# Kernel tuning notes

Hardware: AMD Instinct MI355X
Metric: run time of the kernel (lower is better)

Reference implementation:

```python
import jax, jax.numpy as jnp
import numpy as np

TEMPERATURE = 0.05
EPS = 1e-8  # torch.cosine_similarity eps


def setup_inputs() -> dict:
    key = jax.random.key(0)
    k1, k2 = jax.random.split(key)
    N, D = 8192, 256
    text_embeddings = jax.random.normal(k1, (N, D), dtype=jnp.float32)
    text_pos_embeddings = jax.random.normal(k2, (N, D), dtype=jnp.float32)
    return {"text_embeddings": text_embeddings, "text_pos_embeddings": text_pos_embeddings}


def reference(text_embeddings, text_pos_embeddings):
    # cosine similarity via normalize + single GEMM (same math as broadcasted
    # torch.cosine_similarity, which clamps norms at eps)
    a_norm = jnp.maximum(jnp.linalg.norm(text_embeddings, axis=-1, keepdims=True), EPS)
    b_norm = jnp.maximum(jnp.linalg.norm(text_pos_embeddings, axis=-1, keepdims=True), EPS)
    a = text_embeddings / a_norm  # [N, D]
    b = text_pos_embeddings / b_norm  # [N, D]
    sim = jnp.einsum("nd,md->nm", a, b) / TEMPERATURE  # [N, N]
    # cross-entropy with labels = arange(N): mean over rows of -log_softmax diag
    logp = jax.nn.log_softmax(sim, axis=-1)
    loss = -jnp.mean(jnp.diagonal(logp))
    return loss
```

## Files before the change

### kernel.cpp

```cpp
#include <hip/hip_runtime.h>
#include <math.h>

#define DIM 256

typedef float f32x4 __attribute__((ext_vector_type(4)));
typedef int   i32x8 __attribute__((ext_vector_type(8)));

__constant__ const float kTempInvLog2e = 20.0f * 1.4426950408889634f;
#define LN2 0.6931471805599453f
#define EPS_NORM 1e-8f
#define SCALE_ONE 0x7F7F7F7Fu

static __device__ inline unsigned f2fp8x4(float4 v, float s) {
    int r = 0;
    r = __builtin_amdgcn_cvt_pk_fp8_f32(v.x * s, v.y * s, r, false);
    r = __builtin_amdgcn_cvt_pk_fp8_f32(v.z * s, v.w * s, r, true);
    return (unsigned)r;
}

static __device__ inline i32x8 mk_frag(uint4 a, uint4 b) {
    i32x8 v;
    v[0] = a.x; v[1] = a.y; v[2] = a.z; v[3] = a.w;
    v[4] = b.x; v[5] = b.y; v[6] = b.z; v[7] = b.w;
    return v;
}

__global__ __launch_bounds__(256) void normpack_kernel(
    const float* __restrict__ A, const float* __restrict__ B,
    unsigned char* __restrict__ Apk, unsigned char* __restrict__ Bpk,
    float* __restrict__ diag, float* __restrict__ rowsum,
    unsigned* __restrict__ counter, int n)
{
    __shared__ uint4 lA[256];
    __shared__ uint4 lB[256];
    const int t = threadIdx.x;
    const int rl = t >> 4;
    const int c16 = t & 15;
    const int r = blockIdx.x * 16 + rl;

    if (blockIdx.x == 0 && t == 0) counter[0] = 0;

    const float4* pa = (const float4*)(A + (size_t)r * DIM + c16 * 16);
    const float4* pb = (const float4*)(B + (size_t)r * DIM + c16 * 16);
    float4 a0 = pa[0], a1 = pa[1], a2 = pa[2], a3 = pa[3];
    float4 b0 = pb[0], b1 = pb[1], b2 = pb[2], b3 = pb[3];

    float ssa = a0.x*a0.x + a0.y*a0.y + a0.z*a0.z + a0.w*a0.w
              + a1.x*a1.x + a1.y*a1.y + a1.z*a1.z + a1.w*a1.w
              + a2.x*a2.x + a2.y*a2.y + a2.z*a2.z + a2.w*a2.w
              + a3.x*a3.x + a3.y*a3.y + a3.z*a3.z + a3.w*a3.w;
    float ssb = b0.x*b0.x + b0.y*b0.y + b0.z*b0.z + b0.w*b0.w
              + b1.x*b1.x + b1.y*b1.y + b1.z*b1.z + b1.w*b1.w
              + b2.x*b2.x + b2.y*b2.y + b2.z*b2.z + b2.w*b2.w
              + b3.x*b3.x + b3.y*b3.y + b3.z*b3.z + b3.w*b3.w;
    float dd  = a0.x*b0.x + a0.y*b0.y + a0.z*b0.z + a0.w*b0.w
              + a1.x*b1.x + a1.y*b1.y + a1.z*b1.z + a1.w*b1.w
              + a2.x*b2.x + a2.y*b2.y + a2.z*b2.z + a2.w*b2.w
              + a3.x*b3.x + a3.y*b3.y + a3.z*b3.z + a3.w*b3.w;
#pragma unroll
    for (int m = 1; m < 16; m <<= 1) {
        ssa += __shfl_xor(ssa, m, 64);
        ssb += __shfl_xor(ssb, m, 64);
        dd  += __shfl_xor(dd, m, 64);
    }
    float na = fmaxf(sqrtf(ssa), EPS_NORM);
    float nb = fmaxf(sqrtf(ssb), EPS_NORM);
    float sa = kTempInvLog2e / na;
    float sb = 1.0f / nb;
    if (c16 == 0) {
        diag[r] = dd / (na * nb) * kTempInvLog2e;
        rowsum[r] = 0.0f;
    }

    const int u = ((c16 >> 3) << 7) + ((c16 & 1) << 6) + rl + ((c16 & 7) >> 1) * 16;
    uint4 ga, gb;
    ga.x = f2fp8x4(a0, sa); ga.y = f2fp8x4(a1, sa);
    ga.z = f2fp8x4(a2, sa); ga.w = f2fp8x4(a3, sa);
    gb.x = f2fp8x4(b0, sb); gb.y = f2fp8x4(b1, sb);
    gb.z = f2fp8x4(b2, sb); gb.w = f2fp8x4(b3, sb);
    lA[u] = ga; lB[u] = gb;
    __syncthreads();

    ((uint4*)Apk)[(size_t)blockIdx.x * 256 + t] = lA[t];
    ((uint4*)Bpk)[(size_t)blockIdx.x * 256 + t] = lB[t];
}

__global__ __launch_bounds__(256, 2) void gemm_lse_kernel(
    const unsigned char* __restrict__ Apk, const unsigned char* __restrict__ Bpk,
    float* __restrict__ rowsum, const float* __restrict__ diag,
    unsigned* __restrict__ counter, float* __restrict__ out, int n)
{
    const int t = threadIdx.x;
    const int lane = t & 63;
    const int w = t >> 6;
    const int c = lane & 15;
    const int q = lane >> 4;

    const int i = blockIdx.x;
    const int split = ((i & 7) << 1) | ((i >> 3) & 1);
    const int rowblk = i >> 4;
    const int rowbase = rowblk * 256 + w * 64;

    i32x8 afrag[4][2];
#pragma unroll
    for (int m = 0; m < 4; ++m) {
        const int AT = rowblk * 16 + w * 4 + m;
#pragma unroll
        for (int kc = 0; kc < 2; ++kc) {
            const char* base = (const char*)Apk + ((size_t)AT * 2 + kc) * 2048 + lane * 16;
            afrag[m][kc] = mk_frag(*(const uint4*)base, *(const uint4*)(base + 1024));
        }
    }
#pragma unroll
    for (int m = 0; m < 4; ++m)
#pragma unroll
        for (int kc = 0; kc < 2; ++kc)
            asm volatile("" : "+v"(afrag[m][kc]));

    float sums[16];
#pragma unroll
    for (int s = 0; s < 16; ++s) sums[s] = 0.0f;

    const char* bb = (const char*)Bpk + (size_t)split * 32 * 4096 + (size_t)lane * 16;

#define LOADT(BUF, IT) do {                                                  \
    _Pragma("unroll") for (int j = 0; j < 8; ++j)                            \
        BUF[j] = *(const uint4*)(bb + (IT) * 8192 + j * 1024);               \
} while (0)

#define STEP(BUF) do {                                                       \
    f32x4 acc[4][2];                                                         \
    _Pragma("unroll") for (int m = 0; m < 4; ++m)                            \
        _Pragma("unroll") for (int nc = 0; nc < 2; ++nc)                     \
            acc[m][nc] = (f32x4){0.f, 0.f, 0.f, 0.f};                        \
    _Pragma("unroll") for (int nc = 0; nc < 2; ++nc)                         \
        _Pragma("unroll") for (int kc = 0; kc < 2; ++kc) {                   \
            i32x8 bf = mk_frag(BUF[nc * 4 + kc * 2], BUF[nc * 4 + kc * 2 + 1]); \
            _Pragma("unroll") for (int m = 0; m < 4; ++m)                    \
                acc[m][nc] = __builtin_amdgcn_mfma_scale_f32_16x16x128_f8f6f4( \
                    afrag[m][kc], bf, acc[m][nc],                            \
                    0, 0, 0, SCALE_ONE, 0, SCALE_ONE);                       \
        }                                                                    \
    _Pragma("unroll") for (int m = 0; m < 4; ++m)                            \
        _Pragma("unroll") for (int nc = 0; nc < 2; ++nc)                     \
            _Pragma("unroll") for (int r = 0; r < 4; ++r)                    \
                sums[m * 4 + r] += __builtin_amdgcn_exp2f(acc[m][nc][r]);    \
} while (0)

    uint4 bufA[8], bufB[8];
    LOADT(bufA, 0);
#pragma unroll
    for (int ip = 0; ip < 8; ++ip) {
        LOADT(bufB, 2 * ip + 1);
        STEP(bufA);
        if (2 * ip + 2 < 16) LOADT(bufA, 2 * ip + 2);
        STEP(bufB);
    }
#undef LOADT
#undef STEP

#pragma unroll
    for (int s = 0; s < 16; ++s) {
        float v = sums[s];
        v += __shfl_xor(v, 1, 64);
        v += __shfl_xor(v, 2, 64);
        v += __shfl_xor(v, 4, 64);
        v += __shfl_xor(v, 8, 64);
        sums[s] = v;
    }
    if (c == 0) {
#pragma unroll
        for (int m = 0; m < 4; ++m)
#pragma unroll
            for (int r = 0; r < 4; ++r)
                atomicAdd(&rowsum[rowbase + m * 16 + q * 4 + r], sums[m * 4 + r]);
    }

    __syncthreads();
    __shared__ unsigned lastFlag;
    __shared__ float red[4];
    if (t == 0) {
        __threadfence();
        lastFlag = (__hip_atomic_fetch_add(counter, 1u, __ATOMIC_ACQ_REL,
                                           __HIP_MEMORY_SCOPE_AGENT)
                    == gridDim.x - 1) ? 1u : 0u;
    }
    __syncthreads();
    if (lastFlag) {
        float local = 0.0f;
        for (int row = t; row < n; row += 256) {
            float rs = __hip_atomic_load(&rowsum[row], __ATOMIC_RELAXED,
                                         __HIP_MEMORY_SCOPE_AGENT);
            local += log2f(rs) - diag[row];
        }
#pragma unroll
        for (int m = 1; m < 64; m <<= 1)
            local += __shfl_xor(local, m, 64);
        if ((t & 63) == 0) red[t >> 6] = local;
        __syncthreads();
        if (t == 0) out[0] = (red[0] + red[1] + red[2] + red[3]) * (LN2 / (float)n);
    }
}

extern "C" void kernel_launch(void* const* d_in, const int* in_sizes, int n_in,
                              void* d_out, int out_size, void* d_ws, size_t ws_size,
                              hipStream_t stream) {
    const int n = in_sizes[0] / DIM;
    const float* A = (const float*)d_in[0];
    const float* B = (const float*)d_in[1];
    float* out = (float*)d_out;

    unsigned char* Apk = (unsigned char*)d_ws;
    unsigned char* Bpk = Apk + (size_t)n * DIM;
    float* rowsum = (float*)(Bpk + (size_t)n * DIM);
    float* diag = rowsum + n;
    unsigned* counter = (unsigned*)(diag + n);

    normpack_kernel<<<n / 16, 256, 0, stream>>>(A, B, Apk, Bpk, diag, rowsum, counter, n);

    gemm_lse_kernel<<<(n / 256) * 16, 256, 0, stream>>>(Apk, Bpk, rowsum, diag, counter, out, n);
}
```

Measured before the change: 108.0 us.

## Split GEMM columns 32 ways and move final reduction to separate kernel

Doubles the column-split count of the fused GEMM+logsumexp kernel so each block handles half as many B tiles, launching twice as many blocks with a higher occupancy hint in launch bounds. The last-block atomic-counter completion scheme is replaced by a separate single-block finale kernel that reduces rowsum and diag into the loss. This is meant to improve load balance and occupancy across CUs and to drop the fence and counter atomic. In exchange it doubles the rowsum atomics and A-fragment reloads, adds a third kernel launch, and the tighter register budget may cause spills.

```diff
diff --git a/kernel.cpp b/kernel.cpp
--- a/kernel.cpp
+++ b/kernel.cpp
@@ -28,8 +28,7 @@
 __global__ __launch_bounds__(256) void normpack_kernel(
     const float* __restrict__ A, const float* __restrict__ B,
     unsigned char* __restrict__ Apk, unsigned char* __restrict__ Bpk,
-    float* __restrict__ diag, float* __restrict__ rowsum,
-    unsigned* __restrict__ counter, int n)
+    float* __restrict__ diag, float* __restrict__ rowsum, int n)
 {
     __shared__ uint4 lA[256];
     __shared__ uint4 lB[256];
@@ -37,8 +36,6 @@
     const int rl = t >> 4;
     const int c16 = t & 15;
     const int r = blockIdx.x * 16 + rl;
-
-    if (blockIdx.x == 0 && t == 0) counter[0] = 0;
 
     const float4* pa = (const float4*)(A + (size_t)r * DIM + c16 * 16);
     const float4* pb = (const float4*)(B + (size_t)r * DIM + c16 * 16);
@@ -85,10 +82,9 @@
     ((uint4*)Bpk)[(size_t)blockIdx.x * 256 + t] = lB[t];
 }
 
-__global__ __launch_bounds__(256, 2) void gemm_lse_kernel(
+__global__ __launch_bounds__(256, 4) void gemm_lse_kernel(
     const unsigned char* __restrict__ Apk, const unsigned char* __restrict__ Bpk,
-    float* __restrict__ rowsum, const float* __restrict__ diag,
-    unsigned* __restrict__ counter, float* __restrict__ out, int n)
+    float* __restrict__ rowsum, int n)
 {
     const int t = threadIdx.x;
     const int lane = t & 63;
@@ -97,8 +93,9 @@
     const int q = lane >> 4;
 
     const int i = blockIdx.x;
-    const int split = ((i & 7) << 1) | ((i >> 3) & 1);
-    const int rowblk = i >> 4;
+    const int j = i >> 3;
+    const int split = ((i & 7) << 2) | (j & 3);
+    const int rowblk = j >> 2;
     const int rowbase = rowblk * 256 + w * 64;
 
     i32x8 afrag[4][2];
@@ -121,11 +118,11 @@
 #pragma unroll
     for (int s = 0; s < 16; ++s) sums[s] = 0.0f;
 
-    const char* bb = (const char*)Bpk + (size_t)split * 32 * 4096 + (size_t)lane * 16;
+    const char* bb = (const char*)Bpk + (size_t)split * 65536 + (size_t)lane * 16;
 
 #define LOADT(BUF, IT) do {                                                  \
-    _Pragma("unroll") for (int j = 0; j < 8; ++j)                            \
-        BUF[j] = *(const uint4*)(bb + (IT) * 8192 + j * 1024);               \
+    _Pragma("unroll") for (int jj = 0; jj < 8; ++jj)                         \
+        BUF[jj] = *(const uint4*)(bb + (IT) * 8192 + jj * 1024);             \
 } while (0)
 
 #define STEP(BUF) do {                                                       \
@@ -150,10 +147,10 @@
     uint4 bufA[8], bufB[8];
     LOADT(bufA, 0);
 #pragma unroll
-    for (int ip = 0; ip < 8; ++ip) {
+    for (int ip = 0; ip < 4; ++ip) {
         LOADT(bufB, 2 * ip + 1);
         STEP(bufA);
-        if (2 * ip + 2 < 16) LOADT(bufA, 2 * ip + 2);
+        if (2 * ip + 2 < 8) LOADT(bufA, 2 * ip + 2);
         STEP(bufB);
     }
 #undef LOADT
@@ -175,31 +172,23 @@
             for (int r = 0; r < 4; ++r)
                 atomicAdd(&rowsum[rowbase + m * 16 + q * 4 + r], sums[m * 4 + r]);
     }
-
+}
+
+__global__ __launch_bounds__(1024) void finale_kernel(
+    const float* __restrict__ rowsum, const float* __restrict__ diag,
+    float* __restrict__ out, int n)
+{
+    __shared__ float red[1024];
+    float local = 0.0f;
+    for (int row = threadIdx.x; row < n; row += 1024)
+        local += log2f(rowsum[row]) - diag[row];
+    red[threadIdx.x] = local;
     __syncthreads();
-    __shared__ unsigned lastFlag;
-    __shared__ float red[4];
-    if (t == 0) {
-        __threadfence();
-        lastFlag = (__hip_atomic_fetch_add(counter, 1u, __ATOMIC_ACQ_REL,
-                                           __HIP_MEMORY_SCOPE_AGENT)
-                    == gridDim.x - 1) ? 1u : 0u;
-    }
-    __syncthreads();
-    if (lastFlag) {
-        float local = 0.0f;
-        for (int row = t; row < n; row += 256) {
-            float rs = __hip_atomic_load(&rowsum[row], __ATOMIC_RELAXED,
-                                         __HIP_MEMORY_SCOPE_AGENT);
-            local += log2f(rs) - diag[row];
-        }
-#pragma unroll
-        for (int m = 1; m < 64; m <<= 1)
-            local += __shfl_xor(local, m, 64);
-        if ((t & 63) == 0) red[t >> 6] = local;
+    for (int off = 512; off > 0; off >>= 1) {
+        if (threadIdx.x < off) red[threadIdx.x] += red[threadIdx.x + off];
         __syncthreads();
-        if (t == 0) out[0] = (red[0] + red[1] + red[2] + red[3]) * (LN2 / (float)n);
-    }
+    }
+    if (threadIdx.x == 0) out[0] = red[0] * (LN2 / (float)n);
 }
 
 extern "C" void kernel_launch(void* const* d_in, const int* in_sizes, int n_in,
@@ -214,9 +203,10 @@
     unsigned char* Bpk = Apk + (size_t)n * DIM;
     float* rowsum = (float*)(Bpk + (size_t)n * DIM);
     float* diag = rowsum + n;
-    unsigned* counter = (unsigned*)(diag + n);
-
-    normpack_kernel<<<n / 16, 256, 0, stream>>>(A, B, Apk, Bpk, diag, rowsum, counter, n);
-
-    gemm_lse_kernel<<<(n / 256) * 16, 256, 0, stream>>>(Apk, Bpk, rowsum, diag, counter, out, n);
-}
+
+    normpack_kernel<<<n / 16, 256, 0, stream>>>(A, B, Apk, Bpk, diag, rowsum, n);
+
+    gemm_lse_kernel<<<(n / 256) * 32, 256, 0, stream>>>(Apk, Bpk, rowsum, n);
+
+    finale_kernel<<<1, 1024, 0, stream>>>(rowsum, diag, out, n);
+}
```

New measurement: 202.9 us. 1.88x slower.
